# Kernel tuning notes

Measured on AMD Instinct MI355X. Metric: run time of the kernel, lower is better.

The kernel has to match this reference:

```python
import jax, jax.numpy as jnp
import numpy as np

# segment-boundary byte set (matches ByteContextEncoder.SEGMENT_BYTES)
_SEG_BYTES = b' \t\n\r.,;:!?()[]{}"\'' + b'+-*/=<>|&^~%@#$\\'
_SEP_TABLE = np.zeros(256, dtype=bool)
_SEP_TABLE[list(_SEG_BYTES)] = True

B, T, D, H, L = 4, 2048, 512, 8, 4
HID = 4 * D          # SwiGLU hidden dim
DH = D // H          # head dim
EPS = 1e-6
ALPHA = 0.5
ROPE_BASE = 10000.0


def setup_inputs() -> dict:
    key = jax.random.key(0)
    ks = jax.random.split(key, 10)
    std = D ** -0.5
    tokens = jax.random.randint(ks[0], (B, T), 0, 256)
    embed = jax.random.normal(ks[1], (256, D), dtype=jnp.float32) * std
    wq = jax.random.normal(ks[2], (L, D, D), dtype=jnp.float32) * std
    wk = jax.random.normal(ks[3], (L, D, D), dtype=jnp.float32) * std
    wv = jax.random.normal(ks[4], (L, D, D), dtype=jnp.float32) * std
    wo = jax.random.normal(ks[5], (L, D, D), dtype=jnp.float32) * std
    w1 = jax.random.normal(ks[6], (L, HID, D), dtype=jnp.float32) * std  # gate proj
    w3 = jax.random.normal(ks[7], (L, HID, D), dtype=jnp.float32) * std  # up proj
    w2 = jax.random.normal(ks[8], (L, D, HID), dtype=jnp.float32) * (HID ** -0.5)  # down proj
    attn_norm_w = jnp.ones((L, D), dtype=jnp.float32)
    ffn_norm_w = jnp.ones((L, D), dtype=jnp.float32)
    final_norm_w = jnp.ones((D,), dtype=jnp.float32)
    return {"tokens": tokens, "embed": embed, "attn_norm_w": attn_norm_w,
            "wq": wq, "wk": wk, "wv": wv, "wo": wo,
            "ffn_norm_w": ffn_norm_w, "w1": w1, "w2": w2, "w3": w3,
            "final_norm_w": final_norm_w}


def _rmsnorm(x, w):
    return x * jax.lax.rsqrt(jnp.mean(x * x, axis=-1, keepdims=True) + EPS) * w


def _rope_tables():
    inv = 1.0 / (ROPE_BASE ** (jnp.arange(0, DH, 2, dtype=jnp.float32) / DH))  # (DH/2,)
    ang = jnp.arange(T, dtype=jnp.float32)[:, None] * inv[None, :]             # (T, DH/2)
    return jnp.cos(ang), jnp.sin(ang)


def _apply_rope(x, cos, sin):
    # x: (B, T, H, DH); rotate interleaved pairs
    x1, x2 = x[..., ::2], x[..., 1::2]
    c = cos[None, :, None, :]
    s = sin[None, :, None, :]
    r1 = x1 * c - x2 * s
    r2 = x1 * s + x2 * c
    return jnp.stack([r1, r2], axis=-1).reshape(x.shape)


def _attention(x, Wq, Wk, Wv, Wo, cos, sin):
    q = (x @ Wq.T).reshape(B, T, H, DH)
    k = (x @ Wk.T).reshape(B, T, H, DH)
    v = (x @ Wv.T).reshape(B, T, H, DH)
    q = _apply_rope(q, cos, sin)
    k = _apply_rope(k, cos, sin)
    scores = jnp.einsum('bthd,bshd->bhts', q, k) / jnp.sqrt(jnp.float32(DH))
    a = jax.nn.softmax(scores, axis=-1)  # bidirectional (causal=False)
    o = jnp.einsum('bhts,bshd->bthd', a, v).reshape(B, T, D)
    return o @ Wo.T


def _swiglu(x, W1, W2, W3):
    return (jax.nn.silu(x @ W1.T) * (x @ W3.T)) @ W2.T


def _segment_pool(h, tokens):
    # segment ids via cumsum of separator indicator; per-batch offset b*(T+1)
    sep = jnp.asarray(_SEP_TABLE)[tokens].astype(jnp.int32)          # (B, T)
    seg = jnp.cumsum(sep, axis=1) + jnp.arange(B, dtype=jnp.int32)[:, None] * (T + 1)
    flat_s = seg.reshape(B * T)
    flat_h = h.reshape(B * T, D)
    nseg = B * (T + 1)
    seg_sum = jax.ops.segment_sum(flat_h, flat_s, num_segments=nseg)  # (nseg, D)
    seg_cnt = jax.ops.segment_sum(jnp.ones((B * T,), h.dtype), flat_s, num_segments=nseg)
    seg_cnt = jnp.maximum(seg_cnt, 1.0)
    seg_mean = (seg_sum / seg_cnt[:, None])[flat_s].reshape(B, T, D)
    return ALPHA * h + (1.0 - ALPHA) * seg_mean


def reference(tokens, embed, attn_norm_w, wq, wk, wv, wo, ffn_norm_w, w1, w2, w3, final_norm_w):
    tokens = jnp.clip(tokens, 0, 255)
    x = embed[tokens]  # (B, T, D); dropout=0 -> identity
    cos, sin = _rope_tables()
    for l in range(L):
        x = x + _attention(_rmsnorm(x, attn_norm_w[l]), wq[l], wk[l], wv[l], wo[l], cos, sin)
        x = x + _swiglu(_rmsnorm(x, ffn_norm_w[l]), w1[l], w2[l], w3[l])
    x = _rmsnorm(x, final_norm_w)
    return _segment_pool(x, tokens)
```

## Files before the change

kernel.cpp:

```cpp
#include <hip/hip_runtime.h>
#include <math.h>

#define Bq 4
#define Tt 2048
#define Dd 512
#define Hh 8
#define Ll 4
#define HIDN 2048
#define DHd 64
#define BT (Bq*Tt)
#define BTD ((size_t)BT*Dd)

typedef __attribute__((ext_vector_type(8))) __bf16 bf16x8;
typedef __attribute__((ext_vector_type(4))) __bf16 bf16x4;
typedef __attribute__((ext_vector_type(2))) __bf16 bf16x2;
typedef __attribute__((ext_vector_type(4))) float f32x4;

static __device__ __forceinline__ int is_sep(int t) {
    const unsigned long long w0 = 0xFC00FFFF00002600ULL;
    const unsigned long long w1 = 0x7800000078000001ULL;
    if (t < 64)  return (int)((w0 >> t) & 1ULL);
    if (t < 128) return (int)((w1 >> (t - 64)) & 1ULL);
    return 0;
}

static __device__ __forceinline__ void gload16(const void* g, void* l) {
    __builtin_amdgcn_global_load_lds(
        (const __attribute__((address_space(1))) void*)g,
        (__attribute__((address_space(3))) void*)l, 16, 0, 0);
}

__global__ void embed_kernel(const int* __restrict__ tokens, const float* __restrict__ embed,
                             float* __restrict__ x) {
    size_t idx = (size_t)blockIdx.x * blockDim.x + threadIdx.x;
    if (idx >= BTD / 4) return;
    size_t row = idx >> 7;
    int tk = tokens[row];
    tk = tk < 0 ? 0 : (tk > 255 ? 255 : tk);
    const float4* src = (const float4*)(embed + (size_t)tk * Dd);
    ((float4*)x)[idx] = src[idx & 127];
}

__global__ void rope_table_kernel(float* __restrict__ cosb, float* __restrict__ sinb) {
    int idx = blockIdx.x * blockDim.x + threadIdx.x;
    if (idx >= Tt * 32) return;
    int t = idx >> 5, j = idx & 31;
    float inv = powf(10000.0f, -(2.0f * j) / 64.0f);
    float ang = (float)t * inv;
    cosb[idx] = cosf(ang);
    sinb[idx] = sinf(ang);
}

__global__ void cvt_bf16_kernel(const float* __restrict__ in, __bf16* __restrict__ out, int n8) {
    int i = blockIdx.x * blockDim.x + threadIdx.x;
    if (i >= n8) return;
    const float4* p = (const float4*)(in + (size_t)i * 8);
    float4 a = p[0], b = p[1];
    bf16x8 o8;
    o8[0] = (__bf16)a.x; o8[1] = (__bf16)a.y; o8[2] = (__bf16)a.z; o8[3] = (__bf16)a.w;
    o8[4] = (__bf16)b.x; o8[5] = (__bf16)b.y; o8[6] = (__bf16)b.z; o8[7] = (__bf16)b.w;
    *(bf16x8*)(out + (size_t)i * 8) = o8;
}

__global__ void cvt_qkv_kernel(const float* __restrict__ wq, const float* __restrict__ wk,
                               const float* __restrict__ wv, __bf16* __restrict__ out) {
    int i = blockIdx.x * blockDim.x + threadIdx.x;
    if (i >= 393216) return;
    int l = i / 98304;
    int r = i - l * 98304;
    int t = r >> 15;
    int pos8 = r & 32767;
    const float* src = (t == 0 ? wq : (t == 1 ? wk : wv)) + (size_t)l * 262144 + (size_t)pos8 * 8;
    float4 a = *(const float4*)src;
    float4 b = *(const float4*)(src + 4);
    bf16x8 o8;
    o8[0] = (__bf16)a.x; o8[1] = (__bf16)a.y; o8[2] = (__bf16)a.z; o8[3] = (__bf16)a.w;
    o8[4] = (__bf16)b.x; o8[5] = (__bf16)b.y; o8[6] = (__bf16)b.z; o8[7] = (__bf16)b.w;
    *(bf16x8*)(out + (size_t)i * 8) = o8;
}

__global__ void rmsnorm_kernel(const float* __restrict__ x, const float* __restrict__ w,
                               float* __restrict__ y) {
    int row = blockIdx.x * 4 + (threadIdx.x >> 6);
    int lane = threadIdx.x & 63;
    const float* xr = x + (size_t)row * Dd + lane * 8;
    float4 a = *(const float4*)xr;
    float4 b = *(const float4*)(xr + 4);
    float ss = a.x * a.x + a.y * a.y + a.z * a.z + a.w * a.w
             + b.x * b.x + b.y * b.y + b.z * b.z + b.w * b.w;
    #pragma unroll
    for (int off = 1; off < 64; off <<= 1) ss += __shfl_xor(ss, off);
    float scale = rsqrtf(ss * (1.0f / Dd) + 1e-6f);
    const float* wr = w + lane * 8;
    float4 wa = *(const float4*)wr;
    float4 wb = *(const float4*)(wr + 4);
    float* yo = y + (size_t)row * Dd + lane * 8;
    *(float4*)yo = make_float4(a.x * scale * wa.x, a.y * scale * wa.y,
                               a.z * scale * wa.z, a.w * scale * wa.w);
    *(float4*)(yo + 4) = make_float4(b.x * scale * wb.x, b.y * scale * wb.y,
                                     b.z * scale * wb.z, b.w * scale * wb.w);
}

__global__ void rmsnorm_bf16_kernel(const float* __restrict__ x, const float* __restrict__ w,
                                    __bf16* __restrict__ y) {
    int row = blockIdx.x * 4 + (threadIdx.x >> 6);
    int lane = threadIdx.x & 63;
    const float* xr = x + (size_t)row * Dd + lane * 8;
    float4 a = *(const float4*)xr;
    float4 b = *(const float4*)(xr + 4);
    float ss = a.x * a.x + a.y * a.y + a.z * a.z + a.w * a.w
             + b.x * b.x + b.y * b.y + b.z * b.z + b.w * b.w;
    #pragma unroll
    for (int off = 1; off < 64; off <<= 1) ss += __shfl_xor(ss, off);
    float scale = rsqrtf(ss * (1.0f / Dd) + 1e-6f);
    const float* wr = w + lane * 8;
    float4 wa = *(const float4*)wr;
    float4 wb = *(const float4*)(wr + 4);
    bf16x8 o;
    o[0] = (__bf16)(a.x * scale * wa.x); o[1] = (__bf16)(a.y * scale * wa.y);
    o[2] = (__bf16)(a.z * scale * wa.z); o[3] = (__bf16)(a.w * scale * wa.w);
    o[4] = (__bf16)(b.x * scale * wb.x); o[5] = (__bf16)(b.y * scale * wb.y);
    o[6] = (__bf16)(b.z * scale * wb.z); o[7] = (__bf16)(b.w * scale * wb.w);
    *(bf16x8*)(y + (size_t)row * Dd + lane * 8) = o;
}

template<int EPI>
__global__ __launch_bounds__(256) void gemm_bt_mfma(
    const __bf16* __restrict__ A, const __bf16* __restrict__ Bw,
    const float* __restrict__ res, void* __restrict__ Cout,
    int N, int K,
    const float* __restrict__ cosb, const float* __restrict__ sinb) {
    __shared__ __align__(16) __bf16 lds[2][2][128 * 32];
    const int tid = threadIdx.x;
    const int w = tid >> 6, lane = tid & 63;
    const int l15 = lane & 15, g4 = lane >> 4;
    const int wr = w >> 1, wc = w & 1;
    const int bm = blockIdx.y * 128, bn = blockIdx.x * 128;
    const int lrow = lane >> 2, lc8 = (lane & 3) * 8;
    const int chunk0 = w * 2;

    f32x4 acc[4][4];
    #pragma unroll
    for (int m = 0; m < 4; m++)
        #pragma unroll
        for (int n = 0; n < 4; n++) acc[m][n] = (f32x4){0.f, 0.f, 0.f, 0.f};

    auto stage = [&](int buf, int k0) {
        #pragma unroll
        for (int c = 0; c < 2; c++) {
            int chunk = chunk0 + c;
            const __bf16* ga = A + (size_t)(bm + chunk * 16 + lrow) * K + k0 + lc8;
            gload16(ga, &lds[buf][0][chunk * 512]);
            const __bf16* gb = Bw + (size_t)(bn + chunk * 16 + lrow) * K + k0 + lc8;
            gload16(gb, &lds[buf][1][chunk * 512]);
        }
    };

    stage(0, 0);
    __syncthreads();
    const int NT = K >> 5;
    int cur = 0;
    for (int t = 0; t < NT; t++) {
        if (t + 1 < NT) stage(cur ^ 1, (t + 1) << 5);
        const __bf16* Al = &lds[cur][0][0];
        const __bf16* Bl = &lds[cur][1][0];
        bf16x8 af[4], bfr[4];
        #pragma unroll
        for (int m = 0; m < 4; m++)
            af[m] = *(const bf16x8*)&Al[(wr * 64 + m * 16 + l15) * 32 + g4 * 8];
        #pragma unroll
        for (int n = 0; n < 4; n++)
            bfr[n] = *(const bf16x8*)&Bl[(wc * 64 + n * 16 + l15) * 32 + g4 * 8];
        #pragma unroll
        for (int m = 0; m < 4; m++)
            #pragma unroll
            for (int n = 0; n < 4; n++)
                acc[m][n] = __builtin_amdgcn_mfma_f32_16x16x32_bf16(af[m], bfr[n], acc[m][n], 0, 0, 0);
        __syncthreads();
        cur ^= 1;
    }

    #pragma unroll
    for (int m = 0; m < 4; m++)
        #pragma unroll
        for (int n = 0; n < 4; n++)
            #pragma unroll
            for (int r = 0; r < 4; r++) {
                size_t row = bm + wr * 64 + m * 16 + g4 * 4 + r;
                int col = bn + wc * 64 + n * 16 + l15;
                if (EPI == 0) {
                    ((__bf16*)Cout)[row * N + col] = (__bf16)acc[m][n][r];
                } else if (EPI == 1) {
                    ((float*)Cout)[row * N + col] = acc[m][n][r] + res[row * N + col];
                } else {
                    float vv = acc[m][n][r];
                    float vp = __shfl_xor(vv, 1);
                    if (col < 1024) {
                        int trow = (int)(row & (Tt - 1));
                        int p = (col & 63) >> 1;
                        float c = cosb[trow * 32 + p];
                        float s = sinb[trow * 32 + p];
                        float x1 = (col & 1) ? vp : vv;
                        float x2 = (col & 1) ? vv : vp;
                        float rot = (col & 1) ? (x1 * s + x2 * c) : (x1 * c - x2 * s);
                        if (col < 512) rot *= 0.18033688011112043f;
                        vv = rot;
                    }
                    ((__bf16*)Cout)[(size_t)(col >> 9) * BTD + row * 512 + (col & 511)] =
                        (__bf16)vv;
                }
            }
}

__global__ __launch_bounds__(256) void gemm_bt_mfma64(
    const __bf16* __restrict__ A, const __bf16* __restrict__ Bw,
    const float* __restrict__ res, float* __restrict__ Cout,
    int N, int K) {
    __shared__ __align__(16) __bf16 lds[2][2][64 * 32];
    const int tid = threadIdx.x;
    const int w = tid >> 6, lane = tid & 63;
    const int l15 = lane & 15, g4 = lane >> 4;
    const int wr = w >> 1, wc = w & 1;
    const int bm = blockIdx.y * 64, bn = blockIdx.x * 64;
    const int srow = tid >> 2, scol8 = (tid & 3) * 8;

    f32x4 acc[2][2];
    #pragma unroll
    for (int m = 0; m < 2; m++)
        #pragma unroll
        for (int n = 0; n < 2; n++) acc[m][n] = (f32x4){0.f, 0.f, 0.f, 0.f};

    auto stage = [&](int buf, int k0) {
        gload16(A + (size_t)(bm + srow) * K + k0 + scol8, &lds[buf][0][srow * 32 + scol8]);
        gload16(Bw + (size_t)(bn + srow) * K + k0 + scol8, &lds[buf][1][srow * 32 + scol8]);
    };

    stage(0, 0);
    __syncthreads();
    const int NT = K >> 5;
    int cur = 0;
    for (int t = 0; t < NT; t++) {
        if (t + 1 < NT) stage(cur ^ 1, (t + 1) << 5);
        const __bf16* Al = &lds[cur][0][0];
        const __bf16* Bl = &lds[cur][1][0];
        bf16x8 af[2], bfr[2];
        #pragma unroll
        for (int m = 0; m < 2; m++)
            af[m] = *(const bf16x8*)&Al[(wr * 32 + m * 16 + l15) * 32 + g4 * 8];
        #pragma unroll
        for (int n = 0; n < 2; n++)
            bfr[n] = *(const bf16x8*)&Bl[(wc * 32 + n * 16 + l15) * 32 + g4 * 8];
        #pragma unroll
        for (int m = 0; m < 2; m++)
            #pragma unroll
            for (int n = 0; n < 2; n++)
                acc[m][n] = __builtin_amdgcn_mfma_f32_16x16x32_bf16(af[m], bfr[n], acc[m][n], 0, 0, 0);
        __syncthreads();
        cur ^= 1;
    }

    #pragma unroll
    for (int m = 0; m < 2; m++)
        #pragma unroll
        for (int n = 0; n < 2; n++)
            #pragma unroll
            for (int r = 0; r < 4; r++) {
                size_t row = bm + wr * 32 + m * 16 + g4 * 4 + r;
                int col = bn + wc * 32 + n * 16 + l15;
                Cout[row * N + col] = acc[m][n][r] + res[row * N + col];
            }
}

__global__ __launch_bounds__(256) void gemm_swiglu_mfma(
    const __bf16* __restrict__ A, const __bf16* __restrict__ W1,
    const __bf16* __restrict__ W3, __bf16* __restrict__ G,
    int N, int K) {
    __shared__ __align__(16) __bf16 lds[2][3][128 * 32];
    const int tid = threadIdx.x;
    const int w = tid >> 6, lane = tid & 63;
    const int l15 = lane & 15, g4 = lane >> 4;
    const int wr = w >> 1, wc = w & 1;
    const int bm = blockIdx.y * 128, bn = blockIdx.x * 128;
    const int lrow = lane >> 2, lc8 = (lane & 3) * 8;
    const int chunk0 = w * 2;

    f32x4 acc1[4][4], acc3[4][4];
    #pragma unroll
    for (int m = 0; m < 4; m++)
        #pragma unroll
        for (int n = 0; n < 4; n++) {
            acc1[m][n] = (f32x4){0.f, 0.f, 0.f, 0.f};
            acc3[m][n] = (f32x4){0.f, 0.f, 0.f, 0.f};
        }

    auto stage = [&](int buf, int k0) {
        #pragma unroll
        for (int c = 0; c < 2; c++) {
            int chunk = chunk0 + c;
            const __bf16* ga = A + (size_t)(bm + chunk * 16 + lrow) * K + k0 + lc8;
            gload16(ga, &lds[buf][0][chunk * 512]);
            const __bf16* g1 = W1 + (size_t)(bn + chunk * 16 + lrow) * K + k0 + lc8;
            gload16(g1, &lds[buf][1][chunk * 512]);
            const __bf16* g3 = W3 + (size_t)(bn + chunk * 16 + lrow) * K + k0 + lc8;
            gload16(g3, &lds[buf][2][chunk * 512]);
        }
    };

    stage(0, 0);
    __syncthreads();
    const int NT = K >> 5;
    int cur = 0;
    for (int t = 0; t < NT; t++) {
        if (t + 1 < NT) stage(cur ^ 1, (t + 1) << 5);
        const __bf16* Al = &lds[cur][0][0];
        const __bf16* B1 = &lds[cur][1][0];
        const __bf16* B3 = &lds[cur][2][0];
        bf16x8 af[4];
        #pragma unroll
        for (int m = 0; m < 4; m++)
            af[m] = *(const bf16x8*)&Al[(wr * 64 + m * 16 + l15) * 32 + g4 * 8];
        #pragma unroll
        for (int n = 0; n < 4; n++) {
            bf16x8 b1 = *(const bf16x8*)&B1[(wc * 64 + n * 16 + l15) * 32 + g4 * 8];
            bf16x8 b3 = *(const bf16x8*)&B3[(wc * 64 + n * 16 + l15) * 32 + g4 * 8];
            #pragma unroll
            for (int m = 0; m < 4; m++) {
                acc1[m][n] = __builtin_amdgcn_mfma_f32_16x16x32_bf16(af[m], b1, acc1[m][n], 0, 0, 0);
                acc3[m][n] = __builtin_amdgcn_mfma_f32_16x16x32_bf16(af[m], b3, acc3[m][n], 0, 0, 0);
            }
        }
        __syncthreads();
        cur ^= 1;
    }

    #pragma unroll
    for (int m = 0; m < 4; m++)
        #pragma unroll
        for (int n = 0; n < 4; n++)
            #pragma unroll
            for (int r = 0; r < 4; r++) {
                size_t row = bm + wr * 64 + m * 16 + g4 * 4 + r;
                size_t col = bn + wc * 64 + n * 16 + l15;
                float a1 = acc1[m][n][r];
                float sig = 1.0f / (1.0f + __expf(-a1));
                G[row * N + col] = (__bf16)(a1 * sig * acc3[m][n][r]);
            }
}

__global__ __launch_bounds__(512) void attn_mfma_kernel(
    const __bf16* __restrict__ q, const __bf16* __restrict__ k,
    const __bf16* __restrict__ v, __bf16* __restrict__ o) {
    __shared__ __align__(16) __bf16 Ks[2][64][72];
    __shared__ __align__(16) unsigned int VtW[2][64 * 36];

    int tid = threadIdx.x;
    int w = tid >> 6;
    int lane = tid & 63;
    int l15 = lane & 15;
    int g = lane >> 4;
    int i = blockIdx.x;
    int xcd = i & 7, jj = i >> 3;
    int bh = xcd * 4 + (jj >> 4);
    int qtile = jj & 15;
    int b = bh >> 3, h = bh & 7;
    int qbase = qtile * 128;

    const __bf16* qp = q + (size_t)b * Tt * Dd + (size_t)h * DHd;
    const __bf16* kp = k + (size_t)b * Tt * Dd + (size_t)h * DHd;
    const __bf16* vp = v + (size_t)b * Tt * Dd + (size_t)h * DHd;

    int krow = tid >> 3;
    int ksc8 = (tid & 7) * 8;
    int r2v  = tid >> 4;
    int sc4  = (tid & 15) * 4;
    int sgrow = 8 * (l15 >> 2) + (l15 & 3);

    bf16x8 qa[2];
    {
        const __bf16* qrow = qp + (size_t)(qbase + w * 16 + l15) * Dd;
        qa[0] = *(const bf16x8*)(qrow + g * 8);
        qa[1] = *(const bf16x8*)(qrow + 32 + g * 8);
    }

    f32x4 oacc[4];
    #pragma unroll
    for (int i2 = 0; i2 < 4; i2++) oacc[i2] = (f32x4){0.f, 0.f, 0.f, 0.f};
    float mrun = -1e30f;
    float lrun = 0.f;

    bf16x8 kreg;
    bf16x4 vreg0, vreg1;
    auto ldkv = [&](int t) {
        size_t base = (size_t)(t * 64) * Dd;
        kreg  = *(const bf16x8*)(kp + base + (size_t)krow * Dd + ksc8);
        vreg0 = *(const bf16x4*)(vp + base + (size_t)(2 * r2v) * Dd + sc4);
        vreg1 = *(const bf16x4*)(vp + base + (size_t)(2 * r2v + 1) * Dd + sc4);
    };
    auto stash = [&](int buf) {
        *(bf16x8*)&Ks[buf][krow][ksc8] = kreg;
        const unsigned short* v0 = (const unsigned short*)&vreg0;
        const unsigned short* v1 = (const unsigned short*)&vreg1;
        #pragma unroll
        for (int j = 0; j < 4; j++) {
            int d = sc4 + j;
            int col = (r2v + 4 * ((d >> 3) & 7)) & 31;
            unsigned int word = (unsigned int)v0[j] | ((unsigned int)v1[j] << 16);
            VtW[buf][d * 36 + col] = word;
        }
    };

    const int NT = Tt / 64;
    ldkv(0);
    stash(0);
    ldkv(1);
    __syncthreads();

    for (int t = 0; t < NT; t++) {
        int cur = t & 1;
        f32x4 s4[4];
        __builtin_amdgcn_s_setprio(1);
        #pragma unroll
        for (int c = 0; c < 4; c++) {
            int row = sgrow + (c & 1) * 32 + (c >> 1) * 4;
            s4[c] = (f32x4){0.f, 0.f, 0.f, 0.f};
            bf16x8 kb0 = *(const bf16x8*)&Ks[cur][row][g * 8];
            s4[c] = __builtin_amdgcn_mfma_f32_16x16x32_bf16(kb0, qa[0], s4[c], 0, 0, 0);
            bf16x8 kb1 = *(const bf16x8*)&Ks[cur][row][32 + g * 8];
            s4[c] = __builtin_amdgcn_mfma_f32_16x16x32_bf16(kb1, qa[1], s4[c], 0, 0, 0);
        }
        __builtin_amdgcn_s_setprio(0);

        if (t + 1 < NT) stash(cur ^ 1);
        if (t + 2 < NT) ldkv(t + 2);

        float lm = fmaxf(fmaxf(fmaxf(s4[0][0], s4[0][1]), fmaxf(s4[0][2], s4[0][3])),
                         fmaxf(fmaxf(s4[1][0], s4[1][1]), fmaxf(s4[1][2], s4[1][3])));
        lm = fmaxf(lm, fmaxf(fmaxf(s4[2][0], s4[2][1]), fmaxf(s4[2][2], s4[2][3])));
        lm = fmaxf(lm, fmaxf(fmaxf(s4[3][0], s4[3][1]), fmaxf(s4[3][2], s4[3][3])));
        bool near = (lm - mrun <= 8.f);
        if (!__all((int)near)) {
            float tm = fmaxf(lm, __shfl_xor(lm, 16));
            tm = fmaxf(tm, __shfl_xor(tm, 32));
            float mnew = fmaxf(mrun, tm);
            float alpha = exp2f(mrun - mnew);
            mrun = mnew;
            lrun *= alpha;
            float ar[4];
            #pragma unroll
            for (int r = 0; r < 4; r++) ar[r] = __shfl(alpha, 20 * g + r);
            #pragma unroll
            for (int d2 = 0; d2 < 4; d2++)
                #pragma unroll
                for (int r = 0; r < 4; r++) oacc[d2][r] *= ar[r];
        }
        float psum = 0.f;
        bf16x8 pa0, pa1;
        #pragma unroll
        for (int cc = 0; cc < 2; cc++)
            #pragma unroll
            for (int r = 0; r < 4; r++) {
                float e0 = exp2f(s4[2 * cc][r] - mrun);
                float e1 = exp2f(s4[2 * cc + 1][r] - mrun);
                psum += e0 + e1;
                pa0[cc * 4 + r] = (__bf16)e0;
                pa1[cc * 4 + r] = (__bf16)e1;
            }
        lrun += psum;

        __builtin_amdgcn_s_setprio(1);
        #pragma unroll
        for (int d2 = 0; d2 < 4; d2++) {
            int d = d2 * 16 + l15;
            int rot = ((2 * d2 + (l15 >> 3)) & 7) * 4;
            const unsigned int* vrow = VtW[cur] + d * 36;
            bf16x8 vb0 = *(const bf16x8*)(vrow + ((4 * g + rot) & 31));
            bf16x8 vb1 = *(const bf16x8*)(vrow + ((16 + 4 * g + rot) & 31));
            oacc[d2] = __builtin_amdgcn_mfma_f32_16x16x32_bf16(pa0, vb0, oacc[d2], 0, 0, 0);
            oacc[d2] = __builtin_amdgcn_mfma_f32_16x16x32_bf16(pa1, vb1, oacc[d2], 0, 0, 0);
        }
        __builtin_amdgcn_s_setprio(0);

        __syncthreads();
    }

    lrun += __shfl_xor(lrun, 16);
    lrun += __shfl_xor(lrun, 32);
    float lr[4];
    #pragma unroll
    for (int r = 0; r < 4; r++) lr[r] = __shfl(lrun, 20 * g + r);

    __bf16* op = o + (size_t)b * Tt * Dd + (size_t)h * DHd;
    #pragma unroll
    for (int d2 = 0; d2 < 4; d2++)
        #pragma unroll
        for (int r = 0; r < 4; r++)
            op[(size_t)(qbase + w * 16 + g * 4 + r) * Dd + d2 * 16 + l15] =
                (__bf16)(oacc[d2][r] / lr[r]);
}

__global__ void seg_scan_kernel(const int* __restrict__ tokens, int* __restrict__ segid) {
    int b = blockIdx.x;
    int tid = threadIdx.x;
    const int* trow = tokens + (size_t)b * Tt;
    int base = tid * 8;
    int inc[8];
    int run = 0;
    #pragma unroll
    for (int i = 0; i < 8; i++) {
        int tk = trow[base + i];
        tk = tk < 0 ? 0 : (tk > 255 ? 255 : tk);
        run += is_sep(tk);
        inc[i] = run;
    }
    __shared__ int part[256];
    part[tid] = run;
    __syncthreads();
    for (int off = 1; off < 256; off <<= 1) {
        int vv = (tid >= off) ? part[tid - off] : 0;
        __syncthreads();
        part[tid] += vv;
        __syncthreads();
    }
    int exc = part[tid] - run;
    #pragma unroll
    for (int i = 0; i < 8; i++)
        segid[(size_t)b * Tt + base + i] = exc + inc[i] + b * (Tt + 1);
}

__global__ void seg_cnt_kernel(const int* __restrict__ segid, float* __restrict__ cnt) {
    int i = blockIdx.x * blockDim.x + threadIdx.x;
    if (i < BT) atomicAdd(&cnt[segid[i]], 1.0f);
}

__global__ void seg_accum_kernel(const float* __restrict__ h, const int* __restrict__ segid,
                                 float* __restrict__ segsum) {
    size_t idx = (size_t)blockIdx.x * blockDim.x + threadIdx.x;
    if (idx >= BTD) return;
    size_t row = idx >> 9;
    int d = idx & 511;
    atomicAdd(&segsum[(size_t)segid[row] * Dd + d], h[idx]);
}

__global__ void seg_final_kernel(const float* __restrict__ h, const float* __restrict__ segsum,
                                 const float* __restrict__ cnt, const int* __restrict__ segid,
                                 float* __restrict__ out) {
    size_t idx = (size_t)blockIdx.x * blockDim.x + threadIdx.x;
    if (idx >= BTD) return;
    size_t row = idx >> 9;
    int d = idx & 511;
    int s = segid[row];
    float mean = segsum[(size_t)s * Dd + d] / fmaxf(cnt[s], 1.0f);
    out[idx] = 0.5f * h[idx] + 0.5f * mean;
}

extern "C" void kernel_launch(void* const* d_in, const int* in_sizes, int n_in,
                              void* d_out, int out_size, void* d_ws, size_t ws_size,
                              hipStream_t stream) {
    const int*   tokens       = (const int*)d_in[0];
    const float* embedw       = (const float*)d_in[1];
    const float* attn_norm_w  = (const float*)d_in[2];
    const float* wq           = (const float*)d_in[3];
    const float* wk           = (const float*)d_in[4];
    const float* wv           = (const float*)d_in[5];
    const float* wo           = (const float*)d_in[6];
    const float* ffn_norm_w   = (const float*)d_in[7];
    const float* w1           = (const float*)d_in[8];
    const float* w2           = (const float*)d_in[9];
    const float* w3           = (const float*)d_in[10];
    const float* final_norm_w = (const float*)d_in[11];
    float* out = (float*)d_out;
    float* ws  = (float*)d_ws;

    float*  x    = ws;
    __bf16* qkvo = (__bf16*)(ws + BTD);
    __bf16* qb   = qkvo;
    __bf16* kb   = qkvo + BTD;
    __bf16* vb   = qkvo + 2 * BTD;
    __bf16* obuf = qkvo + 3 * BTD;
    __bf16* gbuf = qkvo;
    float*  segsum = ws;
    float*  hfin   = ws + 2 * BTD;
    __bf16* xnb  = (__bf16*)(ws + 3 * BTD);
    __bf16* wb   = (__bf16*)(ws + 3 * BTD + BTD / 2);
    float*  cosb = ws + 3 * BTD + BTD / 2 + 8388608;
    float*  sinb = cosb + (size_t)Tt * 32;
    float*  segcnt = sinb + (size_t)Tt * 32;
    int*    segid  = (int*)(segcnt + Bq * (Tt + 1));

    __bf16* wqkvb = wb;
    __bf16* wob = wb + 3145728;
    __bf16* w1b = wb + 4194304;
    __bf16* w3b = wb + 8388608;
    __bf16* w2b = wb + 12582912;

    cvt_qkv_kernel<<<1536, 256, 0, stream>>>(wq, wk, wv, wqkvb);
    cvt_bf16_kernel<<<512, 256, 0, stream>>>(wo, wob, 131072);
    cvt_bf16_kernel<<<2048, 256, 0, stream>>>(w1, w1b, 524288);
    cvt_bf16_kernel<<<2048, 256, 0, stream>>>(w3, w3b, 524288);
    cvt_bf16_kernel<<<2048, 256, 0, stream>>>(w2, w2b, 524288);

    embed_kernel<<<(int)((BTD / 4 + 255) / 256), 256, 0, stream>>>(tokens, embedw, x);
    rope_table_kernel<<<(Tt * 32 + 255) / 256, 256, 0, stream>>>(cosb, sinb);

    dim3 gqkv(12, 64);
    dim3 g64(8, 128);
    dim3 gs(16, 64);
    dim3 ga(512);
    int grms = BT / 4;

    for (int l = 0; l < Ll; l++) {
        size_t oDD = (size_t)l * Dd * Dd;
        size_t oHD = (size_t)l * HIDN * Dd;
        rmsnorm_bf16_kernel<<<grms, 256, 0, stream>>>(x, attn_norm_w + (size_t)l * Dd, xnb);
        gemm_bt_mfma<2><<<gqkv, 256, 0, stream>>>(xnb, wqkvb + (size_t)l * 786432, nullptr, qb,
                                                  1536, Dd, cosb, sinb);
        attn_mfma_kernel<<<ga, 512, 0, stream>>>(qb, kb, vb, obuf);
        gemm_bt_mfma64<<<g64, 256, 0, stream>>>(obuf, wob + oDD, x, x, Dd, Dd);
        rmsnorm_bf16_kernel<<<grms, 256, 0, stream>>>(x, ffn_norm_w + (size_t)l * Dd, xnb);
        gemm_swiglu_mfma<<<gs, 256, 0, stream>>>(xnb, w1b + oHD, w3b + oHD, gbuf, HIDN, Dd);
        gemm_bt_mfma64<<<g64, 256, 0, stream>>>(gbuf, w2b + oHD, x, x, Dd, HIDN);
    }

    rmsnorm_kernel<<<grms, 256, 0, stream>>>(x, final_norm_w, hfin);

    hipMemsetAsync(segsum, 0, (size_t)Bq * (Tt + 1) * Dd * sizeof(float), stream);
    hipMemsetAsync(segcnt, 0, (size_t)Bq * (Tt + 1) * sizeof(float), stream);
    seg_scan_kernel<<<Bq, 256, 0, stream>>>(tokens, segid);
    seg_cnt_kernel<<<(BT + 255) / 256, 256, 0, stream>>>(segid, segcnt);
    seg_accum_kernel<<<(int)((BTD + 255) / 256), 256, 0, stream>>>(hfin, segid, segsum);
    seg_final_kernel<<<(int)((BTD + 255) / 256), 256, 0, stream>>>(hfin, segsum, segcnt, segid, out);
}
```

Measured before the change: 986.1 us.

## Fuse final rmsnorm with segment accumulation and merge weight-conversion launches

Folds the final RMSNorm into a kernel that writes the normalized row in place and atomically adds it into the segment sums. This removes the separate hfin buffer and the full pass over it. Segment counts are now accumulated inside the scan kernel using run-length merged atomics, and the four fp32-to-bf16 weight conversions are combined into one launch. The tail kernels launch fewer times and move less data, at the cost of dependence on contiguous weight buffer offsets and on atomic contention patterns.

```diff
diff --git a/kernel.cpp b/kernel.cpp
--- a/kernel.cpp
+++ b/kernel.cpp
@@ -51,15 +51,22 @@
     sinb[idx] = sinf(ang);
 }
 
-__global__ void cvt_bf16_kernel(const float* __restrict__ in, __bf16* __restrict__ out, int n8) {
+__global__ void cvt_w_kernel(const float* __restrict__ wo, const float* __restrict__ w1,
+                             const float* __restrict__ w3, const float* __restrict__ w2,
+                             __bf16* __restrict__ dst) {
     int i = blockIdx.x * blockDim.x + threadIdx.x;
-    if (i >= n8) return;
-    const float4* p = (const float4*)(in + (size_t)i * 8);
-    float4 a = p[0], b = p[1];
+    if (i >= 1703936) return;
+    const float* src;
+    if (i < 131072)       src = wo + (size_t)i * 8;
+    else if (i < 655360)  src = w1 + (size_t)(i - 131072) * 8;
+    else if (i < 1179648) src = w3 + (size_t)(i - 655360) * 8;
+    else                  src = w2 + (size_t)(i - 1179648) * 8;
+    float4 a = *(const float4*)src;
+    float4 b = *(const float4*)(src + 4);
     bf16x8 o8;
     o8[0] = (__bf16)a.x; o8[1] = (__bf16)a.y; o8[2] = (__bf16)a.z; o8[3] = (__bf16)a.w;
     o8[4] = (__bf16)b.x; o8[5] = (__bf16)b.y; o8[6] = (__bf16)b.z; o8[7] = (__bf16)b.w;
-    *(bf16x8*)(out + (size_t)i * 8) = o8;
+    *(bf16x8*)(dst + (size_t)i * 8) = o8;
 }
 
 __global__ void cvt_qkv_kernel(const float* __restrict__ wq, const float* __restrict__ wk,
@@ -79,28 +86,6 @@
     *(bf16x8*)(out + (size_t)i * 8) = o8;
 }
 
-__global__ void rmsnorm_kernel(const float* __restrict__ x, const float* __restrict__ w,
-                               float* __restrict__ y) {
-    int row = blockIdx.x * 4 + (threadIdx.x >> 6);
-    int lane = threadIdx.x & 63;
-    const float* xr = x + (size_t)row * Dd + lane * 8;
-    float4 a = *(const float4*)xr;
-    float4 b = *(const float4*)(xr + 4);
-    float ss = a.x * a.x + a.y * a.y + a.z * a.z + a.w * a.w
-             + b.x * b.x + b.y * b.y + b.z * b.z + b.w * b.w;
-    #pragma unroll
-    for (int off = 1; off < 64; off <<= 1) ss += __shfl_xor(ss, off);
-    float scale = rsqrtf(ss * (1.0f / Dd) + 1e-6f);
-    const float* wr = w + lane * 8;
-    float4 wa = *(const float4*)wr;
-    float4 wb = *(const float4*)(wr + 4);
-    float* yo = y + (size_t)row * Dd + lane * 8;
-    *(float4*)yo = make_float4(a.x * scale * wa.x, a.y * scale * wa.y,
-                               a.z * scale * wa.z, a.w * scale * wa.w);
-    *(float4*)(yo + 4) = make_float4(b.x * scale * wb.x, b.y * scale * wb.y,
-                                     b.z * scale * wb.z, b.w * scale * wb.w);
-}
-
 __global__ void rmsnorm_bf16_kernel(const float* __restrict__ x, const float* __restrict__ w,
                                     __bf16* __restrict__ y) {
     int row = blockIdx.x * 4 + (threadIdx.x >> 6);
@@ -122,6 +107,33 @@
     o[4] = (__bf16)(b.x * scale * wb.x); o[5] = (__bf16)(b.y * scale * wb.y);
     o[6] = (__bf16)(b.z * scale * wb.z); o[7] = (__bf16)(b.w * scale * wb.w);
     *(bf16x8*)(y + (size_t)row * Dd + lane * 8) = o;
+}
+
+__global__ void rmsnorm_seg_kernel(float* __restrict__ x, const float* __restrict__ w,
+                                   const int* __restrict__ segid, float* __restrict__ segsum) {
+    int row = blockIdx.x * 4 + (threadIdx.x >> 6);
+    int lane = threadIdx.x & 63;
+    float* xr = x + (size_t)row * Dd + lane * 8;
+    float4 a = *(const float4*)xr;
+    float4 b = *(const float4*)(xr + 4);
+    float ss = a.x * a.x + a.y * a.y + a.z * a.z + a.w * a.w
+             + b.x * b.x + b.y * b.y + b.z * b.z + b.w * b.w;
+    #pragma unroll
+    for (int off = 1; off < 64; off <<= 1) ss += __shfl_xor(ss, off);
+    float scale = rsqrtf(ss * (1.0f / Dd) + 1e-6f);
+    const float* wr = w + lane * 8;
+    float4 wa = *(const float4*)wr;
+    float4 wb = *(const float4*)(wr + 4);
+    float o[8];
+    o[0] = a.x * scale * wa.x; o[1] = a.y * scale * wa.y;
+    o[2] = a.z * scale * wa.z; o[3] = a.w * scale * wa.w;
+    o[4] = b.x * scale * wb.x; o[5] = b.y * scale * wb.y;
+    o[6] = b.z * scale * wb.z; o[7] = b.w * scale * wb.w;
+    *(float4*)xr = make_float4(o[0], o[1], o[2], o[3]);
+    *(float4*)(xr + 4) = make_float4(o[4], o[5], o[6], o[7]);
+    float* srow = segsum + (size_t)segid[row] * Dd + lane * 8;
+    #pragma unroll
+    for (int j = 0; j < 8; j++) atomicAdd(&srow[j], o[j]);
 }
 
 template<int EPI>
@@ -498,7 +510,8 @@
                 (__bf16)(oacc[d2][r] / lr[r]);
 }
 
-__global__ void seg_scan_kernel(const int* __restrict__ tokens, int* __restrict__ segid) {
+__global__ void seg_scan_kernel(const int* __restrict__ tokens, int* __restrict__ segid,
+                                float* __restrict__ cnt) {
     int b = blockIdx.x;
     int tid = threadIdx.x;
     const int* trow = tokens + (size_t)b * Tt;
@@ -522,23 +535,20 @@
         __syncthreads();
     }
     int exc = part[tid] - run;
-    #pragma unroll
-    for (int i = 0; i < 8; i++)
-        segid[(size_t)b * Tt + base + i] = exc + inc[i] + b * (Tt + 1);
-}
-
-__global__ void seg_cnt_kernel(const int* __restrict__ segid, float* __restrict__ cnt) {
-    int i = blockIdx.x * blockDim.x + threadIdx.x;
-    if (i < BT) atomicAdd(&cnt[segid[i]], 1.0f);
-}
-
-__global__ void seg_accum_kernel(const float* __restrict__ h, const int* __restrict__ segid,
-                                 float* __restrict__ segsum) {
-    size_t idx = (size_t)blockIdx.x * blockDim.x + threadIdx.x;
-    if (idx >= BTD) return;
-    size_t row = idx >> 9;
-    int d = idx & 511;
-    atomicAdd(&segsum[(size_t)segid[row] * Dd + d], h[idx]);
+    int sid[8];
+    #pragma unroll
+    for (int i = 0; i < 8; i++) {
+        sid[i] = exc + inc[i] + b * (Tt + 1);
+        segid[(size_t)b * Tt + base + i] = sid[i];
+    }
+    int curid = sid[0];
+    float c = 1.0f;
+    #pragma unroll
+    for (int i = 1; i < 8; i++) {
+        if (sid[i] == curid) c += 1.0f;
+        else { atomicAdd(&cnt[curid], c); curid = sid[i]; c = 1.0f; }
+    }
+    atomicAdd(&cnt[curid], c);
 }
 
 __global__ void seg_final_kernel(const float* __restrict__ h, const float* __restrict__ segsum,
@@ -578,8 +588,7 @@
     __bf16* vb   = qkvo + 2 * BTD;
     __bf16* obuf = qkvo + 3 * BTD;
     __bf16* gbuf = qkvo;
-    float*  segsum = ws;
-    float*  hfin   = ws + 2 * BTD;
+    float*  segsum = ws + BTD;
     __bf16* xnb  = (__bf16*)(ws + 3 * BTD);
     __bf16* wb   = (__bf16*)(ws + 3 * BTD + BTD / 2);
     float*  cosb = ws + 3 * BTD + BTD / 2 + 8388608;
@@ -594,10 +603,7 @@
     __bf16* w2b = wb + 12582912;
 
     cvt_qkv_kernel<<<1536, 256, 0, stream>>>(wq, wk, wv, wqkvb);
-    cvt_bf16_kernel<<<512, 256, 0, stream>>>(wo, wob, 131072);
-    cvt_bf16_kernel<<<2048, 256, 0, stream>>>(w1, w1b, 524288);
-    cvt_bf16_kernel<<<2048, 256, 0, stream>>>(w3, w3b, 524288);
-    cvt_bf16_kernel<<<2048, 256, 0, stream>>>(w2, w2b, 524288);
+    cvt_w_kernel<<<6656, 256, 0, stream>>>(wo, w1, w3, w2, wob);
 
     embed_kernel<<<(int)((BTD / 4 + 255) / 256), 256, 0, stream>>>(tokens, embedw, x);
     rope_table_kernel<<<(Tt * 32 + 255) / 256, 256, 0, stream>>>(cosb, sinb);
@@ -621,12 +627,9 @@
         gemm_bt_mfma64<<<g64, 256, 0, stream>>>(gbuf, w2b + oHD, x, x, Dd, HIDN);
     }
 
-    rmsnorm_kernel<<<grms, 256, 0, stream>>>(x, final_norm_w, hfin);
-
     hipMemsetAsync(segsum, 0, (size_t)Bq * (Tt + 1) * Dd * sizeof(float), stream);
     hipMemsetAsync(segcnt, 0, (size_t)Bq * (Tt + 1) * sizeof(float), stream);
-    seg_scan_kernel<<<Bq, 256, 0, stream>>>(tokens, segid);
-    seg_cnt_kernel<<<(BT + 255) / 256, 256, 0, stream>>>(segid, segcnt);
-    seg_accum_kernel<<<(int)((BTD + 255) / 256), 256, 0, stream>>>(hfin, segid, segsum);
-    seg_final_kernel<<<(int)((BTD + 255) / 256), 256, 0, stream>>>(hfin, segsum, segcnt, segid, out);
-}
+    seg_scan_kernel<<<Bq, 256, 0, stream>>>(tokens, segid, segcnt);
+    rmsnorm_seg_kernel<<<grms, 256, 0, stream>>>(x, final_norm_w, segid, segsum);
+    seg_final_kernel<<<(int)((BTD + 255) / 256), 256, 0, stream>>>(x, segsum, segcnt, segid, out);
+}
```

Measured after the change: 1.080 ms. 1.1x slower.
